# Performance work log

Measured on AMD Instinct MI355X. Metric: run time of the kernel, lower is better.

The kernel has to match this reference:

```python
import jax, jax.numpy as jnp
import numpy as np

N = 20000          # nodes
E = 320000         # directed edges (self-loops added in reference)
F_IN = 128         # input node features
HEADS = 8
HID = 64           # per-head hidden channels
G = 64             # graphs in the batch
NUM_CLASSES = 10
NEG_SLOPE = 0.2    # PyG GATConv LeakyReLU slope


def _gat_layer(x, src, dst, W, a_src, a_dst, bias, n_nodes):
    """PyG-style GATConv: messages flow src->dst, softmax over incoming edges."""
    H, C = a_src.shape
    h = (x @ W).reshape(n_nodes, H, C)                     # [N,H,C]
    asrc = jnp.einsum('nhc,hc->nh', h, a_src)              # [N,H]
    adst = jnp.einsum('nhc,hc->nh', h, a_dst)              # [N,H]
    e = jax.nn.leaky_relu(asrc[src] + adst[dst], NEG_SLOPE)  # [Etot,H]
    emax = jax.ops.segment_max(e, dst, num_segments=n_nodes)  # [N,H]
    ee = jnp.exp(e - emax[dst])
    denom = jax.ops.segment_sum(ee, dst, num_segments=n_nodes)
    alpha = ee / (denom[dst] + 1e-16)                      # [Etot,H]
    out = jax.ops.segment_sum(h[src] * alpha[:, :, None], dst, num_segments=n_nodes)
    return out.reshape(n_nodes, H * C) + bias


def setup_inputs() -> dict:
    key = jax.random.key(0)
    ks = jax.random.split(key, 10)
    x = jax.random.normal(ks[0], (N, F_IN), jnp.float32)
    edge_index = jax.random.randint(ks[1], (2, E), 0, N, jnp.int32)
    batch = jnp.sort(jax.random.randint(ks[2], (N,), 0, G, jnp.int32))
    # layer 1: F_IN -> HEADS*HID (concat)
    W1 = jax.random.normal(ks[3], (F_IN, HEADS * HID), jnp.float32) / np.float32(np.sqrt(F_IN))
    a_src1 = jax.random.normal(ks[4], (HEADS, HID), jnp.float32) / np.float32(np.sqrt(HID))
    a_dst1 = jax.random.normal(ks[5], (HEADS, HID), jnp.float32) / np.float32(np.sqrt(HID))
    b1 = jnp.zeros((HEADS * HID,), jnp.float32)
    # layer 2: HEADS*HID -> NUM_CLASSES (1 head)
    W2 = jax.random.normal(ks[6], (HEADS * HID, NUM_CLASSES), jnp.float32) / np.float32(np.sqrt(HEADS * HID))
    a_src2 = jax.random.normal(ks[7], (1, NUM_CLASSES), jnp.float32) / np.float32(np.sqrt(NUM_CLASSES))
    a_dst2 = jax.random.normal(ks[8], (1, NUM_CLASSES), jnp.float32) / np.float32(np.sqrt(NUM_CLASSES))
    b2 = jnp.zeros((NUM_CLASSES,), jnp.float32)
    return {"x": x, "edge_index": edge_index, "batch": batch,
            "W1": W1, "a_src1": a_src1, "a_dst1": a_dst1, "b1": b1,
            "W2": W2, "a_src2": a_src2, "a_dst2": a_dst2, "b2": b2}


def reference(x, edge_index, batch, W1, a_src1, a_dst1, b1, W2, a_src2, a_dst2, b2):
    n = x.shape[0]
    loop = jnp.arange(n, dtype=edge_index.dtype)   # add_self_loops=True (PyG default)
    src = jnp.concatenate([edge_index[0], loop])
    dst = jnp.concatenate([edge_index[1], loop])
    h = jax.nn.elu(_gat_layer(x, src, dst, W1, a_src1, a_dst1, b1, n))
    h = _gat_layer(h, src, dst, W2, a_src2, a_dst2, b2, n)
    # PowerMeanAggregation with default p=1.0 == mean pooling per graph
    sums = jax.ops.segment_sum(h, batch, num_segments=G)                    # [G,NC]
    counts = jax.ops.segment_sum(jnp.ones((n, 1), h.dtype), batch, num_segments=G)
    return sums / jnp.maximum(counts, 1.0)
```

## Files before the change

kernel.cpp:

```cpp
#include <hip/hip_runtime.h>
#include <hip/hip_bf16.h>

typedef unsigned short ushort_t;
typedef unsigned int uint_t;
typedef unsigned char uchar_t;

typedef __attribute__((ext_vector_type(8))) short bf16x8;
typedef __attribute__((ext_vector_type(4))) float f32x4;
typedef __attribute__((ext_vector_type(2))) float f32x2;

__device__ __forceinline__ float bf2f(ushort_t u) {
    union { uint_t i; float f; } v; v.i = ((uint_t)u) << 16; return v.f;
}
__device__ __forceinline__ ushort_t f2bf(float f) {
    __hip_bfloat16 h = __float2bfloat16(f);
    ushort_t u; __builtin_memcpy(&u, &h, 2); return u;
}
__device__ __forceinline__ uchar_t f2fp8(float v) {
    int p = __builtin_amdgcn_cvt_pk_fp8_f32(v, v, 0, false);
    return (uchar_t)(p & 0xff);
}
__device__ __forceinline__ float leaky(float v) { return (v > 0.f) ? v : 0.2f * v; }

#define PO_AS1 0
#define PO_AD1 512
#define PO_B1  1024
#define PO_W2  1536
#define PO_AS2 6656
#define PO_AD2 6666
#define PO_B2  6676
#define PTOT   6686

__device__ __forceinline__ bool detect_fp32_local(const ushort_t* __restrict__ xa) {
    __shared__ int cnt;
    if (threadIdx.x == 0) cnt = 0;
    __syncthreads();
    int bad = 0;
    for (int i = threadIdx.x; i < 4096; i += 256) {
        float v = bf2f(xa[i]);
        if (!(fabsf(v) < 1e4f)) bad++;
    }
    if (bad) atomicAdd(&cnt, bad);
    __syncthreads();
    return cnt >= 16;
}

__global__ __launch_bounds__(256) void k_prep(const void* __restrict__ x,
                                              const void* __restrict__ W1,
                                              const void* as1, const void* ad1,
                                              const void* b1, const void* W2,
                                              const void* as2, const void* ad2,
                                              const void* b2,
                                              ushort_t* __restrict__ W1t,
                                              float* __restrict__ prm,
                                              int* __restrict__ deg, int N) {
    int b = blockIdx.x, t = threadIdx.x;
    if (b < 283) {
        bool isf = detect_fp32_local((const ushort_t*)x);
        if (b < 256) {
            int idx = b * 256 + t;
            int n = idx & 511, k = idx >> 9;
            float v = isf ? ((const float*)W1)[k * 512 + n]
                          : bf2f(((const ushort_t*)W1)[k * 512 + n]);
            W1t[n * 128 + k] = f2bf(v);
        } else {
            int i = (b - 256) * 256 + t;
            if (i < PTOT) {
                const void* src; int off;
                if (i < 512)       { src = as1; off = i; }
                else if (i < 1024) { src = ad1; off = i - 512; }
                else if (i < 1536) { src = b1;  off = i - 1024; }
                else if (i < 6656) { src = W2;  off = i - 1536; }
                else if (i < 6666) { src = as2; off = i - 6656; }
                else if (i < 6676) { src = ad2; off = i - 6666; }
                else               { src = b2;  off = i - 6676; }
                prm[i] = isf ? ((const float*)src)[off] : bf2f(((const ushort_t*)src)[off]);
            }
        }
    } else {
        int i = (b - 283) * 256 + t;
        if (i < N) deg[i] = 0;
    }
}

__global__ __launch_bounds__(256) void k_gemm1(const void* __restrict__ xraw,
                                               const ushort_t* __restrict__ w1t,
                                               const float* __restrict__ prm,
                                               uchar_t* __restrict__ h1,
                                               float* __restrict__ asrcf,
                                               float* __restrict__ adstf) {
    int t = threadIdx.x;
    int wave = t >> 6, lane = t & 63;
    int m0 = blockIdx.x * 16;
    bool isf = detect_fp32_local((const ushort_t*)xraw);
    __shared__ ushort_t sA[16 * 128];
    {
        ushort_t tmp[8];
        if (isf) {
            const float4* x4 = (const float4*)((const float*)xraw + (size_t)m0 * 128);
            float4 f0 = x4[2 * t], f1 = x4[2 * t + 1];
            tmp[0] = f2bf(f0.x); tmp[1] = f2bf(f0.y); tmp[2] = f2bf(f0.z); tmp[3] = f2bf(f0.w);
            tmp[4] = f2bf(f1.x); tmp[5] = f2bf(f1.y); tmp[6] = f2bf(f1.z); tmp[7] = f2bf(f1.w);
        } else {
            const uint4* x4 = (const uint4*)((const ushort_t*)xraw + (size_t)m0 * 128);
            uint4 u = x4[t];
            __builtin_memcpy(tmp, &u, 16);
        }
        *reinterpret_cast<uint4*>(&sA[t * 8]) = *reinterpret_cast<uint4*>(tmp);
    }
    __syncthreads();
    int mr = lane & 15, quad = lane >> 4;
    int n0 = wave * 128;
    f32x4 acc[8];
#pragma unroll
    for (int ct = 0; ct < 8; ++ct) acc[ct] = {0.f, 0.f, 0.f, 0.f};
#pragma unroll
    for (int kk = 0; kk < 4; ++kk) {
        bf16x8 a = *reinterpret_cast<const bf16x8*>(&sA[mr * 128 + quad * 8 + kk * 32]);
#pragma unroll
        for (int ct = 0; ct < 8; ++ct) {
            bf16x8 bb = *reinterpret_cast<const bf16x8*>(
                &w1t[(size_t)(n0 + ct * 16 + mr) * 128 + quad * 8 + kk * 32]);
            acc[ct] = __builtin_amdgcn_mfma_f32_16x16x32_bf16(a, bb, acc[ct], 0, 0, 0);
        }
    }
    int col = lane & 15;
#pragma unroll
    for (int hh = 0; hh < 2; ++hh) {
        float Ss[4] = {0.f, 0.f, 0.f, 0.f}, Dd[4] = {0.f, 0.f, 0.f, 0.f};
#pragma unroll
        for (int c4 = 0; c4 < 4; ++c4) {
            int ct = hh * 4 + c4;
            int abscol = n0 + ct * 16 + col;
            float asv = prm[PO_AS1 + abscol];
            float adv = prm[PO_AD1 + abscol];
            float ps[4], pd[4];
#pragma unroll
            for (int r = 0; r < 4; ++r) {
                h1[(size_t)(m0 + quad * 4 + r) * 512 + abscol] = f2fp8(acc[ct][r]);
                ps[r] = acc[ct][r] * asv;
                pd[r] = acc[ct][r] * adv;
            }
#pragma unroll
            for (int off = 1; off <= 8; off <<= 1) {
#pragma unroll
                for (int r = 0; r < 4; ++r) {
                    ps[r] += __shfl_xor(ps[r], off, 64);
                    pd[r] += __shfl_xor(pd[r], off, 64);
                }
            }
#pragma unroll
            for (int r = 0; r < 4; ++r) { Ss[r] += ps[r]; Dd[r] += pd[r]; }
        }
        if (col == 0) {
            int head = 2 * wave + hh;
#pragma unroll
            for (int r = 0; r < 4; ++r) {
                asrcf[(m0 + quad * 4 + r) * 8 + head] = Ss[r];
                adstf[(m0 + quad * 4 + r) * 8 + head] = Dd[r];
            }
        }
    }
}

__global__ void k_hist(const int* __restrict__ ei, int* __restrict__ deg, int E, int Etot) {
    int e = blockIdx.x * 256 + threadIdx.x;
    if (e >= Etot) return;
    int dst = (e < E) ? ei[E + e] : (e - E);
    atomicAdd(&deg[dst], 1);
}

__global__ __launch_bounds__(1024) void k_scan1(const int* __restrict__ deg,
                                                int* __restrict__ rowptr,
                                                int* __restrict__ bsum, int N) {
    int b = blockIdx.x, t = threadIdx.x;
    int lane = t & 63, wv = t >> 6;
    int i = b * 1000 + t;
    int v = (t < 1000 && i < N) ? deg[i] : 0;
    int sv = v;
#pragma unroll
    for (int off = 1; off < 64; off <<= 1) {
        int u = __shfl_up(sv, off, 64);
        if (lane >= off) sv += u;
    }
    __shared__ int wsum[16], woff[16];
    if (lane == 63) wsum[wv] = sv;
    __syncthreads();
    if (t < 16) {
        int s = wsum[t], sc = s;
#pragma unroll
        for (int off = 1; off < 16; off <<= 1) {
            int u = __shfl_up(sc, off, 16);
            if ((t & 15) >= off) sc += u;
        }
        woff[t] = sc - s;
    }
    __syncthreads();
    int inc = sv + woff[wv];
    if (t < 1000 && i < N) rowptr[i + 1] = inc;
    if (t == 1023) bsum[b] = inc;
}

__global__ __launch_bounds__(256) void k_scan3(const int* __restrict__ deg,
                                               const int* __restrict__ bsum,
                                               int* __restrict__ rowptr,
                                               int* __restrict__ cursor, int N) {
    __shared__ int sboffs[20];
    int t = threadIdx.x;
    if (t < 64) {
        int v = (t < 20) ? bsum[t] : 0;
        int sc = v;
#pragma unroll
        for (int off = 1; off < 32; off <<= 1) {
            int u = __shfl_up(sc, off, 64);
            if (t >= off) sc += u;
        }
        if (t < 20) sboffs[t] = sc - v;
    }
    __syncthreads();
    int i = blockIdx.x * 256 + t;
    if (i >= N) return;
    int r = rowptr[i + 1] + sboffs[i / 1000];
    rowptr[i + 1] = r;
    cursor[i] = r - deg[i];
    if (i == 0) rowptr[0] = 0;
}

__global__ void k_scatter(const int* __restrict__ ei, int* __restrict__ cursor,
                          int* __restrict__ csr_src, int E, int Etot) {
    int e = blockIdx.x * 256 + threadIdx.x;
    if (e >= Etot) return;
    int src, dst;
    if (e < E) { src = ei[e]; dst = ei[E + e]; } else { src = dst = e - E; }
    int pos = atomicAdd(&cursor[dst], 1);
    csr_src[pos] = src;
}

__global__ __launch_bounds__(256) void k_agg1(const uchar_t* __restrict__ h1,
                                              const float* __restrict__ asrcf,
                                              const float* __restrict__ adstf,
                                              const int* __restrict__ rowptr,
                                              const int* __restrict__ csr_src,
                                              const float* __restrict__ prm,
                                              float* __restrict__ h2,
                                              float* __restrict__ asrc2f,
                                              float* __restrict__ adst2f) {
    int n = blockIdx.x * 4 + (threadIdx.x >> 6);
    int lane = threadIdx.x & 63;
    int hh = lane >> 3;
    int cb = lane * 8;
    int start = rowptr[n], end = rowptr[n + 1];
    int deg = end - start;
    float adh = adstf[n * 8 + hh];
    float a0 = 0.f, a1 = 0.f, a2 = 0.f, a3 = 0.f, a4 = 0.f, a5 = 0.f, a6 = 0.f, a7 = 0.f;
    float den = 0.f;
    for (int base = 0; base < deg; base += 64) {
        int m = min(64, deg - base);
        int sIdx = csr_src[start + base + min(lane, m - 1)];
        for (int g = 0; g < m; g += 8) {
            int s[8]; float lo[8]; uint2 p[8];
#pragma unroll
            for (int j = 0; j < 8; ++j)
                s[j] = __shfl(sIdx, min(g + j, m - 1), 64);
#pragma unroll
            for (int j = 0; j < 8; ++j)
                lo[j] = asrcf[s[j] * 8 + hh];
#pragma unroll
            for (int j = 0; j < 8; ++j)
                p[j] = *reinterpret_cast<const uint2*>(&h1[(size_t)s[j] * 512 + cb]);
#pragma unroll
            for (int j = 0; j < 8; ++j) {
                float we = (g + j < m) ? __expf(leaky(lo[j] + adh)) : 0.f;
                den += we;
                f32x2 q0 = __builtin_amdgcn_cvt_pk_f32_fp8((int)p[j].x, false);
                f32x2 q1 = __builtin_amdgcn_cvt_pk_f32_fp8((int)p[j].x, true);
                f32x2 q2 = __builtin_amdgcn_cvt_pk_f32_fp8((int)p[j].y, false);
                f32x2 q3 = __builtin_amdgcn_cvt_pk_f32_fp8((int)p[j].y, true);
                a0 += we * q0.x; a1 += we * q0.y;
                a2 += we * q1.x; a3 += we * q1.y;
                a4 += we * q2.x; a5 += we * q2.y;
                a6 += we * q3.x; a7 += we * q3.y;
            }
        }
    }
    float inv = 1.f / (den + 1e-16f);
    float r[8] = {a0, a1, a2, a3, a4, a5, a6, a7};
    float p2[10];
#pragma unroll
    for (int c = 0; c < 10; ++c) p2[c] = 0.f;
#pragma unroll
    for (int j = 0; j < 8; ++j) {
        float rv = r[j] * inv + prm[PO_B1 + cb + j];
        rv = (rv > 0.f) ? rv : expm1f(rv);
#pragma unroll
        for (int c = 0; c < 10; ++c)
            p2[c] += rv * prm[PO_W2 + (cb + j) * 10 + c];
    }
#pragma unroll
    for (int c = 0; c < 10; ++c)
#pragma unroll
        for (int off = 32; off; off >>= 1)
            p2[c] += __shfl_xor(p2[c], off, 64);
    if (lane == 0) {
        float as = 0.f, ad = 0.f;
#pragma unroll
        for (int c = 0; c < 10; ++c) {
            h2[n * 10 + c] = p2[c];
            as += p2[c] * prm[PO_AS2 + c];
            ad += p2[c] * prm[PO_AD2 + c];
        }
        asrc2f[n] = as; adst2f[n] = ad;
    }
}

__global__ __launch_bounds__(256) void k_agg2(const float* __restrict__ h2,
                                              const float* __restrict__ asrc2f,
                                              const float* __restrict__ adst2f,
                                              const int* __restrict__ rowptr,
                                              const int* __restrict__ csr_src,
                                              const float* __restrict__ prm,
                                              float* __restrict__ out2) {
    int n = blockIdx.x * 4 + (threadIdx.x >> 6);
    int l = threadIdx.x & 63;
    int start = rowptr[n], end = rowptr[n + 1];
    float adn = adst2f[n];
    float den = 0.f;
    float oc[10];
#pragma unroll
    for (int c = 0; c < 10; ++c) oc[c] = 0.f;
    int e = start + l;
    int s_cur = (e < end) ? csr_src[e] : 0;
    for (; e < end; ) {
        int e_next = e + 64;
        int s_next = (e_next < end) ? csr_src[e_next] : 0;
        float lo = asrc2f[s_cur];
        const float2* hp = reinterpret_cast<const float2*>(&h2[s_cur * 10]);
        float2 q0 = hp[0], q1 = hp[1], q2 = hp[2], q3 = hp[3], q4 = hp[4];
        float ee = __expf(leaky(lo + adn));
        den += ee;
        oc[0] += ee * q0.x; oc[1] += ee * q0.y;
        oc[2] += ee * q1.x; oc[3] += ee * q1.y;
        oc[4] += ee * q2.x; oc[5] += ee * q2.y;
        oc[6] += ee * q3.x; oc[7] += ee * q3.y;
        oc[8] += ee * q4.x; oc[9] += ee * q4.y;
        e = e_next; s_cur = s_next;
    }
#pragma unroll
    for (int off = 32; off; off >>= 1) {
        den += __shfl_xor(den, off, 64);
#pragma unroll
        for (int c = 0; c < 10; ++c) oc[c] += __shfl_xor(oc[c], off, 64);
    }
    if (l == 0) {
        float inv = 1.f / (den + 1e-16f);
        for (int c = 0; c < 10; ++c) out2[n * 10 + c] = oc[c] * inv + prm[PO_B2 + c];
    }
}

__global__ __launch_bounds__(256) void k_pool(const float* __restrict__ out2,
                                              const int* __restrict__ batch,
                                              const void* __restrict__ x,
                                              void* __restrict__ dout, int N) {
    bool isf = detect_fp32_local((const ushort_t*)x);
    int g = blockIdx.x, t = threadIdx.x;
    __shared__ int s_lo, s_hi;
    __shared__ float sm[256];
    if (t == 0) {
        int lo = 0, hi = N;
        while (lo < hi) { int mid = (lo + hi) >> 1; if (batch[mid] < g) lo = mid + 1; else hi = mid; }
        s_lo = lo;
        int lo2 = lo, hi2 = N;
        while (lo2 < hi2) { int mid = (lo2 + hi2) >> 1; if (batch[mid] < g + 1) lo2 = mid + 1; else hi2 = mid; }
        s_hi = lo2;
    }
    __syncthreads();
    int lo = s_lo, hi = s_hi;
    float acc[10];
#pragma unroll
    for (int c = 0; c < 10; ++c) acc[c] = 0.f;
    for (int i = lo + t; i < hi; i += 256)
#pragma unroll
        for (int c = 0; c < 10; ++c) acc[c] += out2[i * 10 + c];
    float cnt = (float)((hi - lo) > 0 ? (hi - lo) : 1);
    for (int c = 0; c < 10; ++c) {
        sm[t] = acc[c]; __syncthreads();
        for (int off = 128; off; off >>= 1) {
            if (t < off) sm[t] += sm[t + off];
            __syncthreads();
        }
        if (t == 0) {
            float r = sm[0] / cnt;
            if (isf) ((float*)dout)[g * 10 + c] = r;
            else     ((ushort_t*)dout)[g * 10 + c] = f2bf(r);
        }
        __syncthreads();
    }
}

extern "C" void kernel_launch(void* const* d_in, const int* in_sizes, int n_in,
                              void* d_out, int out_size, void* d_ws, size_t ws_size,
                              hipStream_t stream) {
    const void* x   = d_in[0];
    const int* ei   = (const int*)d_in[1];
    const int* batch= (const int*)d_in[2];
    const void* W1  = d_in[3];
    const void* as1 = d_in[4];
    const void* ad1 = d_in[5];
    const void* b1  = d_in[6];
    const void* W2  = d_in[7];
    const void* as2 = d_in[8];
    const void* ad2 = d_in[9];
    const void* b2  = d_in[10];

    constexpr int N = 20000, E = 320000, Etot = E + N;

    char* p = (char*)d_ws;
    auto alloc = [&](size_t bytes) {
        char* r = p; p += (bytes + 255) & ~(size_t)255; return r;
    };
    float* prm      = (float*)alloc((size_t)PTOT * 4);
    ushort_t* w1t   = (ushort_t*)alloc(512 * 128 * 2);
    uchar_t* h1     = (uchar_t*)alloc((size_t)N * 512);
    float* asrc1f   = (float*)alloc((size_t)N * 8 * 4);
    float* adst1f   = (float*)alloc((size_t)N * 8 * 4);
    float* asrc2f   = (float*)alloc((size_t)N * 4);
    float* adst2f   = (float*)alloc((size_t)N * 4);
    float* h2       = (float*)alloc((size_t)N * 10 * 4);
    float* out2     = (float*)alloc((size_t)N * 10 * 4);
    int* deg        = (int*)alloc((size_t)N * 4);
    int* rowptr     = (int*)alloc((size_t)(N + 1) * 4);
    int* cursor     = (int*)alloc((size_t)N * 4);
    int* csr_src    = (int*)alloc((size_t)Etot * 4);
    int* bsum       = (int*)alloc(32 * 4);

    k_prep<<<362, 256, 0, stream>>>(x, W1, as1, ad1, b1, W2, as2, ad2, b2,
                                    w1t, prm, deg, N);
    k_gemm1<<<1250, 256, 0, stream>>>(x, w1t, prm, h1, asrc1f, adst1f);
    k_hist<<<(Etot + 255) / 256, 256, 0, stream>>>(ei, deg, E, Etot);
    k_scan1<<<20, 1024, 0, stream>>>(deg, rowptr, bsum, N);
    k_scan3<<<(N + 255) / 256, 256, 0, stream>>>(deg, bsum, rowptr, cursor, N);
    k_scatter<<<(Etot + 255) / 256, 256, 0, stream>>>(ei, cursor, csr_src, E, Etot);
    k_agg1<<<N / 4, 256, 0, stream>>>(h1, asrc1f, adst1f, rowptr, csr_src, prm,
                                      h2, asrc2f, adst2f);
    k_agg2<<<N / 4, 256, 0, stream>>>(h2, asrc2f, adst2f, rowptr, csr_src, prm, out2);
    k_pool<<<64, 256, 0, stream>>>(out2, batch, x, d_out, N);
}
```

Before: 262.0 us.

## Precompute edge attention weights and split layer-1 aggregation across feature slices

Adds per-edge kernels that compute exp(leaky(asrc+adst)) for both layers into buffers, so the aggregation kernels no longer evaluate exponentials inside the gather loop. Layer-1 aggregation now spreads each node over four blocks, each handling a 128-channel slice, with four edge sub-streams per wave. Partial layer-2 projections are combined via float atomics into a zeroed h2, and a separate kernel computes the layer-2 logits and stores h2 as padded bf16 for aggregation. This exposes more parallelism and shortens the inner loop, at the cost of extra launches, a memset, atomics, and extra global traffic for the weight and dst arrays.

```diff
diff --git a/kernel.cpp b/kernel.cpp
--- a/kernel.cpp
+++ b/kernel.cpp
@@ -227,50 +227,67 @@
 }
 
 __global__ void k_scatter(const int* __restrict__ ei, int* __restrict__ cursor,
-                          int* __restrict__ csr_src, int E, int Etot) {
+                          int* __restrict__ csr_src, int* __restrict__ csr_dst,
+                          int E, int Etot) {
     int e = blockIdx.x * 256 + threadIdx.x;
     if (e >= Etot) return;
     int src, dst;
     if (e < E) { src = ei[e]; dst = ei[E + e]; } else { src = dst = e - E; }
     int pos = atomicAdd(&cursor[dst], 1);
     csr_src[pos] = src;
-}
-
-__global__ __launch_bounds__(256) void k_agg1(const uchar_t* __restrict__ h1,
+    csr_dst[pos] = dst;
+}
+
+__global__ __launch_bounds__(256) void k_wts1(const int* __restrict__ csr_src,
+                                              const int* __restrict__ csr_dst,
                                               const float* __restrict__ asrcf,
                                               const float* __restrict__ adstf,
+                                              float* __restrict__ wts1, int Etot) {
+    int idx = blockIdx.x * 256 + threadIdx.x;
+    if (idx >= Etot * 8) return;
+    int e = idx >> 3, h = idx & 7;
+    int s = csr_src[e], d = csr_dst[e];
+    wts1[idx] = __expf(leaky(asrcf[s * 8 + h] + adstf[d * 8 + h]));
+}
+
+__global__ __launch_bounds__(256) void k_agg1(const uchar_t* __restrict__ h1,
+                                              const float* __restrict__ wts1,
                                               const int* __restrict__ rowptr,
                                               const int* __restrict__ csr_src,
                                               const float* __restrict__ prm,
-                                              float* __restrict__ h2,
-                                              float* __restrict__ asrc2f,
-                                              float* __restrict__ adst2f) {
-    int n = blockIdx.x * 4 + (threadIdx.x >> 6);
-    int lane = threadIdx.x & 63;
-    int hh = lane >> 3;
-    int cb = lane * 8;
+                                              float* __restrict__ h2) {
+    int b = blockIdx.x;
+    int slice = (b & 7) >> 1;
+    int sub = ((b >> 3) << 1) | (b & 1);
+    int wave = threadIdx.x >> 6, lane = threadIdx.x & 63;
+    int n = sub * 4 + wave;
+    int es = lane >> 4;
+    int cl = lane & 15;
+    int cb = slice * 128 + cl * 8;
+    int hh = slice * 2 + (cl >> 3);
     int start = rowptr[n], end = rowptr[n + 1];
     int deg = end - start;
-    float adh = adstf[n * 8 + hh];
     float a0 = 0.f, a1 = 0.f, a2 = 0.f, a3 = 0.f, a4 = 0.f, a5 = 0.f, a6 = 0.f, a7 = 0.f;
     float den = 0.f;
     for (int base = 0; base < deg; base += 64) {
         int m = min(64, deg - base);
         int sIdx = csr_src[start + base + min(lane, m - 1)];
         for (int g = 0; g < m; g += 8) {
-            int s[8]; float lo[8]; uint2 p[8];
-#pragma unroll
-            for (int j = 0; j < 8; ++j)
-                s[j] = __shfl(sIdx, min(g + j, m - 1), 64);
-#pragma unroll
-            for (int j = 0; j < 8; ++j)
-                lo[j] = asrcf[s[j] * 8 + hh];
-#pragma unroll
-            for (int j = 0; j < 8; ++j)
+            int s[2]; float w[2]; uint2 p[2];
+#pragma unroll
+            for (int j = 0; j < 2; ++j) {
+                int idx = g + 4 * j + es;
+                int ce = min(idx, m - 1);
+                s[j] = __shfl(sIdx, ce, 64);
+                float ww = wts1[(size_t)(start + base + ce) * 8 + hh];
+                w[j] = (idx < m) ? ww : 0.f;
+            }
+#pragma unroll
+            for (int j = 0; j < 2; ++j)
                 p[j] = *reinterpret_cast<const uint2*>(&h1[(size_t)s[j] * 512 + cb]);
 #pragma unroll
-            for (int j = 0; j < 8; ++j) {
-                float we = (g + j < m) ? __expf(leaky(lo[j] + adh)) : 0.f;
+            for (int j = 0; j < 2; ++j) {
+                float we = w[j];
                 den += we;
                 f32x2 q0 = __builtin_amdgcn_cvt_pk_f32_fp8((int)p[j].x, false);
                 f32x2 q1 = __builtin_amdgcn_cvt_pk_f32_fp8((int)p[j].x, true);
@@ -283,39 +300,66 @@
             }
         }
     }
+    float a[8] = {a0, a1, a2, a3, a4, a5, a6, a7};
+#pragma unroll
+    for (int off = 16; off <= 32; off <<= 1) {
+        den += __shfl_xor(den, off, 64);
+#pragma unroll
+        for (int j = 0; j < 8; ++j) a[j] += __shfl_xor(a[j], off, 64);
+    }
     float inv = 1.f / (den + 1e-16f);
-    float r[8] = {a0, a1, a2, a3, a4, a5, a6, a7};
     float p2[10];
 #pragma unroll
     for (int c = 0; c < 10; ++c) p2[c] = 0.f;
 #pragma unroll
     for (int j = 0; j < 8; ++j) {
-        float rv = r[j] * inv + prm[PO_B1 + cb + j];
+        float rv = a[j] * inv + prm[PO_B1 + cb + j];
         rv = (rv > 0.f) ? rv : expm1f(rv);
 #pragma unroll
         for (int c = 0; c < 10; ++c)
             p2[c] += rv * prm[PO_W2 + (cb + j) * 10 + c];
     }
 #pragma unroll
-    for (int c = 0; c < 10; ++c)
-#pragma unroll
-        for (int off = 32; off; off >>= 1)
+    for (int off = 1; off <= 8; off <<= 1)
+#pragma unroll
+        for (int c = 0; c < 10; ++c)
             p2[c] += __shfl_xor(p2[c], off, 64);
-    if (lane == 0) {
-        float as = 0.f, ad = 0.f;
-#pragma unroll
-        for (int c = 0; c < 10; ++c) {
-            h2[n * 10 + c] = p2[c];
-            as += p2[c] * prm[PO_AS2 + c];
-            ad += p2[c] * prm[PO_AD2 + c];
-        }
-        asrc2f[n] = as; adst2f[n] = ad;
-    }
-}
-
-__global__ __launch_bounds__(256) void k_agg2(const float* __restrict__ h2,
+    if (lane == 0)
+#pragma unroll
+        for (int c = 0; c < 10; ++c)
+            atomicAdd(&h2[n * 10 + c], p2[c]);
+}
+
+__global__ __launch_bounds__(256) void k_logits2(const float* __restrict__ h2,
+                                                 const float* __restrict__ prm,
+                                                 ushort_t* __restrict__ h2b,
+                                                 float* __restrict__ asrc2f,
+                                                 float* __restrict__ adst2f, int N) {
+    int n = blockIdx.x * 256 + threadIdx.x;
+    if (n >= N) return;
+    float as = 0.f, ad = 0.f;
+#pragma unroll
+    for (int c = 0; c < 10; ++c) {
+        float v = h2[n * 10 + c];
+        h2b[n * 16 + c] = f2bf(v);
+        as += v * prm[PO_AS2 + c];
+        ad += v * prm[PO_AD2 + c];
+    }
+    asrc2f[n] = as; adst2f[n] = ad;
+}
+
+__global__ __launch_bounds__(256) void k_wts2(const int* __restrict__ csr_src,
+                                              const int* __restrict__ csr_dst,
                                               const float* __restrict__ asrc2f,
                                               const float* __restrict__ adst2f,
+                                              float* __restrict__ wts2, int Etot) {
+    int e = blockIdx.x * 256 + threadIdx.x;
+    if (e >= Etot) return;
+    wts2[e] = __expf(leaky(asrc2f[csr_src[e]] + adst2f[csr_dst[e]]));
+}
+
+__global__ __launch_bounds__(256) void k_agg2(const ushort_t* __restrict__ h2b,
+                                              const float* __restrict__ wts2,
                                               const int* __restrict__ rowptr,
                                               const int* __restrict__ csr_src,
                                               const float* __restrict__ prm,
@@ -323,27 +367,24 @@
     int n = blockIdx.x * 4 + (threadIdx.x >> 6);
     int l = threadIdx.x & 63;
     int start = rowptr[n], end = rowptr[n + 1];
-    float adn = adst2f[n];
     float den = 0.f;
     float oc[10];
 #pragma unroll
     for (int c = 0; c < 10; ++c) oc[c] = 0.f;
-    int e = start + l;
-    int s_cur = (e < end) ? csr_src[e] : 0;
-    for (; e < end; ) {
-        int e_next = e + 64;
-        int s_next = (e_next < end) ? csr_src[e_next] : 0;
-        float lo = asrc2f[s_cur];
-        const float2* hp = reinterpret_cast<const float2*>(&h2[s_cur * 10]);
-        float2 q0 = hp[0], q1 = hp[1], q2 = hp[2], q3 = hp[3], q4 = hp[4];
-        float ee = __expf(leaky(lo + adn));
-        den += ee;
-        oc[0] += ee * q0.x; oc[1] += ee * q0.y;
-        oc[2] += ee * q1.x; oc[3] += ee * q1.y;
-        oc[4] += ee * q2.x; oc[5] += ee * q2.y;
-        oc[6] += ee * q3.x; oc[7] += ee * q3.y;
-        oc[8] += ee * q4.x; oc[9] += ee * q4.y;
-        e = e_next; s_cur = s_next;
+    for (int base = start; base < end; base += 64) {
+        int e = base + l;
+        int ce = min(e, end - 1);
+        float w = wts2[ce];
+        if (e >= end) w = 0.f;
+        int s = csr_src[ce];
+        uint4 u0 = *reinterpret_cast<const uint4*>(&h2b[s * 16]);
+        uint_t u1 = *reinterpret_cast<const uint_t*>(&h2b[s * 16 + 8]);
+        den += w;
+        oc[0] += w * bf2f((ushort_t)(u0.x & 0xffff)); oc[1] += w * bf2f((ushort_t)(u0.x >> 16));
+        oc[2] += w * bf2f((ushort_t)(u0.y & 0xffff)); oc[3] += w * bf2f((ushort_t)(u0.y >> 16));
+        oc[4] += w * bf2f((ushort_t)(u0.z & 0xffff)); oc[5] += w * bf2f((ushort_t)(u0.z >> 16));
+        oc[6] += w * bf2f((ushort_t)(u0.w & 0xffff)); oc[7] += w * bf2f((ushort_t)(u0.w >> 16));
+        oc[8] += w * bf2f((ushort_t)(u1 & 0xffff));   oc[9] += w * bf2f((ushort_t)(u1 >> 16));
     }
 #pragma unroll
     for (int off = 32; off; off >>= 1) {
@@ -426,12 +467,18 @@
     float* asrc2f   = (float*)alloc((size_t)N * 4);
     float* adst2f   = (float*)alloc((size_t)N * 4);
     float* h2       = (float*)alloc((size_t)N * 10 * 4);
+    ushort_t* h2b   = (ushort_t*)alloc((size_t)N * 16 * 2);
     float* out2     = (float*)alloc((size_t)N * 10 * 4);
     int* deg        = (int*)alloc((size_t)N * 4);
     int* rowptr     = (int*)alloc((size_t)(N + 1) * 4);
     int* cursor     = (int*)alloc((size_t)N * 4);
     int* csr_src    = (int*)alloc((size_t)Etot * 4);
+    int* csr_dst    = (int*)alloc((size_t)Etot * 4);
+    float* wts1     = (float*)alloc((size_t)Etot * 8 * 4);
+    float* wts2     = (float*)alloc((size_t)Etot * 4);
     int* bsum       = (int*)alloc(32 * 4);
+
+    hipMemsetAsync(h2, 0, (size_t)N * 10 * 4, stream);
 
     k_prep<<<362, 256, 0, stream>>>(x, W1, as1, ad1, b1, W2, as2, ad2, b2,
                                     w1t, prm, deg, N);
@@ -439,9 +486,11 @@
     k_hist<<<(Etot + 255) / 256, 256, 0, stream>>>(ei, deg, E, Etot);
     k_scan1<<<20, 1024, 0, stream>>>(deg, rowptr, bsum, N);
     k_scan3<<<(N + 255) / 256, 256, 0, stream>>>(deg, bsum, rowptr, cursor, N);
-    k_scatter<<<(Etot + 255) / 256, 256, 0, stream>>>(ei, cursor, csr_src, E, Etot);
-    k_agg1<<<N / 4, 256, 0, stream>>>(h1, asrc1f, adst1f, rowptr, csr_src, prm,
-                                      h2, asrc2f, adst2f);
-    k_agg2<<<N / 4, 256, 0, stream>>>(h2, asrc2f, adst2f, rowptr, csr_src, prm, out2);
+    k_scatter<<<(Etot + 255) / 256, 256, 0, stream>>>(ei, cursor, csr_src, csr_dst, E, Etot);
+    k_wts1<<<(Etot * 8 + 255) / 256, 256, 0, stream>>>(csr_src, csr_dst, asrc1f, adst1f, wts1, Etot);
+    k_agg1<<<N, 256, 0, stream>>>(h1, wts1, rowptr, csr_src, prm, h2);
+    k_logits2<<<(N + 255) / 256, 256, 0, stream>>>(h2, prm, h2b, asrc2f, adst2f, N);
+    k_wts2<<<(Etot + 255) / 256, 256, 0, stream>>>(csr_src, csr_dst, asrc2f, adst2f, wts2, Etot);
+    k_agg2<<<N / 4, 256, 0, stream>>>(h2b, wts2, rowptr, csr_src, prm, out2);
     k_pool<<<64, 256, 0, stream>>>(out2, batch, x, d_out, N);
 }
```

After: 417.5 us. 59.4% more time.

## Store h1 head-sliced and split layer-1 aggregation per head with partial combine

Applied to the files above, without the earlier changes.

h1 is now stored head-major, one 64-byte row per node per head, and k_agg1 launches one block per head slice. Each wave processes 8 edges in parallel, with 8 lanes per edge. Partial layer-2 projections go to a per-slice buffer that a new k_comb kernel sums before computing the attention logits. The goal is better cache locality for gathers, since each block touches only one head's contiguous slice, and more memory-level parallelism per wave. The cost is 8x more blocks, repeated rowptr/csr reads per slice, an extra partial-sum buffer and an extra kernel launch.

```diff
diff --git a/kernel.cpp b/kernel.cpp
--- a/kernel.cpp
+++ b/kernel.cpp
@@ -8,6 +8,8 @@
 typedef __attribute__((ext_vector_type(8))) short bf16x8;
 typedef __attribute__((ext_vector_type(4))) float f32x4;
 typedef __attribute__((ext_vector_type(2))) float f32x2;
+
+#define NN 20000
 
 __device__ __forceinline__ float bf2f(ushort_t u) {
     union { uint_t i; float f; } v; v.i = ((uint_t)u) << 16; return v.f;
@@ -132,12 +134,13 @@
         for (int c4 = 0; c4 < 4; ++c4) {
             int ct = hh * 4 + c4;
             int abscol = n0 + ct * 16 + col;
+            int slice = abscol >> 6, within = abscol & 63;
             float asv = prm[PO_AS1 + abscol];
             float adv = prm[PO_AD1 + abscol];
             float ps[4], pd[4];
 #pragma unroll
             for (int r = 0; r < 4; ++r) {
-                h1[(size_t)(m0 + quad * 4 + r) * 512 + abscol] = f2fp8(acc[ct][r]);
+                h1[((size_t)slice * NN + (m0 + quad * 4 + r)) * 64 + within] = f2fp8(acc[ct][r]);
                 ps[r] = acc[ct][r] * asv;
                 pd[r] = acc[ct][r] * adv;
             }
@@ -242,35 +245,40 @@
                                               const int* __restrict__ rowptr,
                                               const int* __restrict__ csr_src,
                                               const float* __restrict__ prm,
-                                              float* __restrict__ h2,
-                                              float* __restrict__ asrc2f,
-                                              float* __restrict__ adst2f) {
-    int n = blockIdx.x * 4 + (threadIdx.x >> 6);
-    int lane = threadIdx.x & 63;
-    int hh = lane >> 3;
-    int cb = lane * 8;
+                                              float* __restrict__ h2part) {
+    int b = blockIdx.x;
+    int slice = b & 7;
+    int wave = threadIdx.x >> 6, lane = threadIdx.x & 63;
+    int n = (b >> 3) * 4 + wave;
+    int es = lane >> 3;
+    int cl = lane & 7;
+    int cb = cl * 8;
+    const uchar_t* hs = h1 + (size_t)slice * NN * 64;
     int start = rowptr[n], end = rowptr[n + 1];
     int deg = end - start;
-    float adh = adstf[n * 8 + hh];
+    float adh = adstf[n * 8 + slice];
     float a0 = 0.f, a1 = 0.f, a2 = 0.f, a3 = 0.f, a4 = 0.f, a5 = 0.f, a6 = 0.f, a7 = 0.f;
     float den = 0.f;
     for (int base = 0; base < deg; base += 64) {
         int m = min(64, deg - base);
+        int ng = (m + 7) >> 3;
         int sIdx = csr_src[start + base + min(lane, m - 1)];
-        for (int g = 0; g < m; g += 8) {
-            int s[8]; float lo[8]; uint2 p[8];
-#pragma unroll
-            for (int j = 0; j < 8; ++j)
-                s[j] = __shfl(sIdx, min(g + j, m - 1), 64);
-#pragma unroll
-            for (int j = 0; j < 8; ++j)
-                lo[j] = asrcf[s[j] * 8 + hh];
-#pragma unroll
-            for (int j = 0; j < 8; ++j)
-                p[j] = *reinterpret_cast<const uint2*>(&h1[(size_t)s[j] * 512 + cb]);
-#pragma unroll
-            for (int j = 0; j < 8; ++j) {
-                float we = (g + j < m) ? __expf(leaky(lo[j] + adh)) : 0.f;
+        int s[8]; float lo[8]; uint2 p[8];
+#pragma unroll
+        for (int j = 0; j < 8; ++j) {
+            int ce = min(j * 8 + es, m - 1);
+            s[j] = __shfl(sIdx, ce, 64);
+        }
+#pragma unroll
+        for (int j = 0; j < 8; ++j)
+            if (j < ng) lo[j] = asrcf[s[j] * 8 + slice];
+#pragma unroll
+        for (int j = 0; j < 8; ++j)
+            if (j < ng) p[j] = *reinterpret_cast<const uint2*>(&hs[(size_t)s[j] * 64 + cb]);
+#pragma unroll
+        for (int j = 0; j < 8; ++j) {
+            if (j < ng) {
+                float we = (j * 8 + es < m) ? __expf(leaky(lo[j] + adh)) : 0.f;
                 den += we;
                 f32x2 q0 = __builtin_amdgcn_cvt_pk_f32_fp8((int)p[j].x, false);
                 f32x2 q1 = __builtin_amdgcn_cvt_pk_f32_fp8((int)p[j].x, true);
@@ -283,34 +291,56 @@
             }
         }
     }
+    float a[8] = {a0, a1, a2, a3, a4, a5, a6, a7};
+#pragma unroll
+    for (int off = 8; off <= 32; off <<= 1) {
+        den += __shfl_xor(den, off, 64);
+#pragma unroll
+        for (int j = 0; j < 8; ++j) a[j] += __shfl_xor(a[j], off, 64);
+    }
     float inv = 1.f / (den + 1e-16f);
-    float r[8] = {a0, a1, a2, a3, a4, a5, a6, a7};
+    int K0 = slice * 64 + cb;
     float p2[10];
 #pragma unroll
     for (int c = 0; c < 10; ++c) p2[c] = 0.f;
 #pragma unroll
     for (int j = 0; j < 8; ++j) {
-        float rv = r[j] * inv + prm[PO_B1 + cb + j];
+        float rv = a[j] * inv + prm[PO_B1 + K0 + j];
         rv = (rv > 0.f) ? rv : expm1f(rv);
 #pragma unroll
         for (int c = 0; c < 10; ++c)
-            p2[c] += rv * prm[PO_W2 + (cb + j) * 10 + c];
-    }
-#pragma unroll
-    for (int c = 0; c < 10; ++c)
-#pragma unroll
-        for (int off = 32; off; off >>= 1)
+            p2[c] += rv * prm[PO_W2 + (K0 + j) * 10 + c];
+    }
+#pragma unroll
+    for (int off = 1; off <= 4; off <<= 1)
+#pragma unroll
+        for (int c = 0; c < 10; ++c)
             p2[c] += __shfl_xor(p2[c], off, 64);
-    if (lane == 0) {
-        float as = 0.f, ad = 0.f;
-#pragma unroll
-        for (int c = 0; c < 10; ++c) {
-            h2[n * 10 + c] = p2[c];
-            as += p2[c] * prm[PO_AS2 + c];
-            ad += p2[c] * prm[PO_AD2 + c];
-        }
-        asrc2f[n] = as; adst2f[n] = ad;
-    }
+    if (lane == 0)
+#pragma unroll
+        for (int c = 0; c < 10; ++c)
+            h2part[((size_t)slice * NN + n) * 10 + c] = p2[c];
+}
+
+__global__ __launch_bounds__(256) void k_comb(const float* __restrict__ h2part,
+                                              const float* __restrict__ prm,
+                                              float* __restrict__ h2,
+                                              float* __restrict__ asrc2f,
+                                              float* __restrict__ adst2f, int N) {
+    int n = blockIdx.x * 256 + threadIdx.x;
+    if (n >= N) return;
+    float as = 0.f, ad = 0.f;
+#pragma unroll
+    for (int c = 0; c < 10; ++c) {
+        float v = 0.f;
+#pragma unroll
+        for (int s = 0; s < 8; ++s)
+            v += h2part[((size_t)s * NN + n) * 10 + c];
+        h2[n * 10 + c] = v;
+        as += v * prm[PO_AS2 + c];
+        ad += v * prm[PO_AD2 + c];
+    }
+    asrc2f[n] = as; adst2f[n] = ad;
 }
 
 __global__ __launch_bounds__(256) void k_agg2(const float* __restrict__ h2,
@@ -412,7 +442,7 @@
     const void* ad2 = d_in[9];
     const void* b2  = d_in[10];
 
-    constexpr int N = 20000, E = 320000, Etot = E + N;
+    constexpr int N = NN, E = 320000, Etot = E + N;
 
     char* p = (char*)d_ws;
     auto alloc = [&](size_t bytes) {
@@ -426,6 +456,7 @@
     float* asrc2f   = (float*)alloc((size_t)N * 4);
     float* adst2f   = (float*)alloc((size_t)N * 4);
     float* h2       = (float*)alloc((size_t)N * 10 * 4);
+    float* h2part   = (float*)alloc((size_t)8 * N * 10 * 4);
     float* out2     = (float*)alloc((size_t)N * 10 * 4);
     int* deg        = (int*)alloc((size_t)N * 4);
     int* rowptr     = (int*)alloc((size_t)(N + 1) * 4);
@@ -440,8 +471,8 @@
     k_scan1<<<20, 1024, 0, stream>>>(deg, rowptr, bsum, N);
     k_scan3<<<(N + 255) / 256, 256, 0, stream>>>(deg, bsum, rowptr, cursor, N);
     k_scatter<<<(Etot + 255) / 256, 256, 0, stream>>>(ei, cursor, csr_src, E, Etot);
-    k_agg1<<<N / 4, 256, 0, stream>>>(h1, asrc1f, adst1f, rowptr, csr_src, prm,
-                                      h2, asrc2f, adst2f);
+    k_agg1<<<N * 8 / 4, 256, 0, stream>>>(h1, asrc1f, adst1f, rowptr, csr_src, prm, h2part);
+    k_comb<<<(N + 255) / 256, 256, 0, stream>>>(h2part, prm, h2, asrc2f, adst2f, N);
     k_agg2<<<N / 4, 256, 0, stream>>>(h2, asrc2f, adst2f, rowptr, csr_src, prm, out2);
     k_pool<<<64, 256, 0, stream>>>(out2, batch, x, d_out, N);
 }
```

Result: slower. 521.0 us (+98.9%).
